# Kernel tuning notes

Hardware: AMD Instinct MI355X
Metric: run time of the kernel (lower is better)

## Reference

```python
import jax, jax.numpy as jnp
import numpy as np

NQ = 8          # n_qubits
NC = 4          # n_cycles of the angle encoder
PI = np.float32(np.pi)
LAYER_QUBITS = [[0, 1, 2, 3, 4, 5, 6, 7], [1, 3, 5, 7]]  # active qubits per conv layer
FINAL_QUBITS = [3, 7]                                    # active after last pooling
CX = jnp.array([[1, 0, 0, 0], [0, 1, 0, 0], [0, 0, 0, 1], [0, 0, 1, 0]], jnp.complex64)


def apply1(psi, U, q):
    """Apply 1-qubit gate U ((2,2) shared or (B,2,2) batched) on qubit q. psi: (B,2,...,2)."""
    psi = jnp.moveaxis(psi, 1 + q, -1)
    if U.ndim == 3:
        psi = jnp.einsum('bij,b...j->b...i', U, psi)
    else:
        psi = jnp.einsum('ij,...j->...i', U, psi)
    return jnp.moveaxis(psi, -1, 1 + q)


def apply2(psi, U, q0, q1):
    """Apply 2-qubit gate U (4,4) on (q0,q1); q0 is the more-significant wire."""
    psi = jnp.moveaxis(psi, (1 + q0, 1 + q1), (-2, -1))
    sh = psi.shape
    psi = jnp.einsum('ij,...j->...i', U, psi.reshape(sh[:-2] + (4,)))
    return jnp.moveaxis(psi.reshape(sh), (-2, -1), (1 + q0, 1 + q1))


def rz_mat(t):
    return jnp.array([[jnp.exp(-0.5j * t), 0.0], [0.0, jnp.exp(0.5j * t)]]).astype(jnp.complex64)


def ry_mat(t):
    c, s = jnp.cos(t / 2), jnp.sin(t / 2)
    return jnp.array([[c, -s], [s, c]]).astype(jnp.complex64)


def crx_mat(t):
    c = jnp.cos(t / 2).astype(jnp.complex64)
    s = jnp.sin(t / 2).astype(jnp.complex64)
    M = jnp.eye(4, dtype=jnp.complex64)
    return M.at[2, 2].set(c).at[3, 3].set(c).at[2, 3].set(-1j * s).at[3, 2].set(-1j * s)


def u3_mat(t, p, l):
    c, s = jnp.cos(t / 2), jnp.sin(t / 2)
    return jnp.array([[c + 0j, -jnp.exp(1j * l) * s],
                      [jnp.exp(1j * p) * s, jnp.exp(1j * (p + l)) * c]]).astype(jnp.complex64)


def expz(psi, q):
    """<Z_q> = P(q=0) - P(q=1)."""
    p = psi.real ** 2 + psi.imag ** 2
    p = jnp.moveaxis(p, 1 + q, 1).reshape(p.shape[0], 2, -1).sum(-1)
    return p[:, 0] - p[:, 1]


def encode(x):
    """Angle-encoding circuit (circuit_builder): NC cycles of RY(x) + CNOT ring."""
    B = x.shape[0]
    psi = jnp.zeros((B, 2 ** NQ), jnp.complex64).at[:, 0].set(1.0).reshape((B,) + (2,) * NQ)
    for c in range(NC):
        ang = x[:, c * NQ:(c + 1) * NQ]
        cc, ss = jnp.cos(ang / 2), jnp.sin(ang / 2)
        for q in range(NQ):
            U = jnp.stack([jnp.stack([cc[:, q], -ss[:, q]], -1),
                           jnp.stack([ss[:, q], cc[:, q]], -1)], -2).astype(jnp.complex64)
            psi = apply1(psi, U, q)
        for q in range(NQ):
            psi = apply2(psi, CX, q, (q + 1) % NQ)
    return psi


def forward(x, rz_p, ry_p, ry2_p, crx_p, u3_p, u3b_p, W1, b1, W2, b2):
    psi0 = encode(x)
    psi1 = psi0  # deepcopy of encoded state for the second feature map
    for layer in range(2):
        aq = LAYER_QUBITS[layer]
        n = len(aq)
        RZp, RYp, RY2p = rz_mat(rz_p[layer]), ry_mat(ry_p[layer]), ry_mat(ry2_p[layer])
        RZm, RZpl = rz_mat(-PI / 2), rz_mat(PI / 2)
        # circuit 1: ZNOTY-style conv blocks, even pairs then odd pairs
        for parity in (0, 1):
            for i in range(parity, n - 1, 2):
                qc, qt = aq[i], aq[i + 1]
                psi0 = apply1(psi0, RZm, qt)
                psi0 = apply2(psi0, CX, qt, qc)
                psi0 = apply1(psi0, RZp, qc)
                psi0 = apply1(psi0, RYp, qt)
                psi0 = apply2(psi0, CX, qc, qt)
                psi0 = apply1(psi0, RY2p, qt)
                psi0 = apply2(psi0, CX, qt, qc)
                psi0 = apply1(psi0, RZpl, qc)
        remain = [aq[i] for i in range(n) if i % 2 == 1]
        U3a = u3_mat(u3_p[layer, 0], u3_p[layer, 1], u3_p[layer, 2])
        for q in remain:
            psi0 = apply1(psi0, U3a, q)
        # circuit 2: CRX conv blocks, even pairs then odd pairs
        CRXp = crx_mat(crx_p[layer])
        for parity in (0, 1):
            for i in range(parity, n - 1, 2):
                psi1 = apply2(psi1, CRXp, aq[i], aq[i + 1])
        U3b = u3_mat(u3b_p[layer, 0], u3b_p[layer, 1], u3b_p[layer, 2])
        for q in remain:
            psi1 = apply1(psi1, U3b, q)
    xv = jnp.stack([expz(psi0, q) for q in FINAL_QUBITS], 1)  # (B,2)
    yv = jnp.stack([expz(psi1, q) for q in FINAL_QUBITS], 1)  # (B,2)
    feat = jnp.concatenate([xv, yv], 1)                       # (B,4)
    h = jnp.tanh(feat @ W1.T + b1)
    return jax.nn.sigmoid(h @ W2.T + b2)


def setup_inputs() -> dict:
    key = jax.random.key(0)
    ks = jax.random.split(key, 12)
    B = 8192
    return {
        'x': jax.random.normal(ks[0], (B, NC * NQ), jnp.float32),
        'rz_p': jax.random.normal(ks[1], (2,), jnp.float32) * 0.5,
        'ry_p': jax.random.normal(ks[2], (2,), jnp.float32) * 0.5,
        'ry2_p': jax.random.normal(ks[3], (2,), jnp.float32) * 0.5,
        'crx_p': jax.random.normal(ks[4], (2,), jnp.float32) * 0.5,
        'u3_p': jax.random.normal(ks[5], (2, 3), jnp.float32) * 0.5,
        'u3b_p': jax.random.normal(ks[6], (2, 3), jnp.float32) * 0.5,
        'W1': jax.random.normal(ks[7], (15, 4), jnp.float32) * 0.4,
        'b1': jax.random.normal(ks[8], (15,), jnp.float32) * 0.1,
        'W2': jax.random.normal(ks[9], (1, 15), jnp.float32) * 0.25,
        'b2': jax.random.normal(ks[10], (1,), jnp.float32) * 0.1,
    }


def reference(x, rz_p, ry_p, ry2_p, crx_p, u3_p, u3b_p, W1, b1, W2, b2):
    return forward(x, rz_p, ry_p, ry2_p, crx_p, u3_p, u3b_p, W1, b1, W2, b2)
```

## Files before the change

kernel.cpp:

```cpp
#include <hip/hip_runtime.h>

#define DEV __device__ __forceinline__


DEV int lpar(int lane, int m) { return __builtin_popcount(lane & m) & 1; }
constexpr int cpar(int v) { return (v ^ (v >> 1) ^ (v >> 2) ^ (v >> 3)) & 1; }

constexpr int TLm(int LM, int SM) { return (LM << 1) | (SM >> 3); }
constexpr int TSm(int SM) { return SM & 7; }

template<int LM, int SM, int LR, int SR>
DEV void ryr(float* p, float gc, float gs, int lane) {
  const float sg0 = lpar(lane, LR) ? gs : -gs;
  const float sg1 = -sg0;
  if constexpr (LM != 0) {
    float t[8];
    #pragma unroll
    for (int s = 0; s < 8; ++s) t[s] = __shfl_xor(p[s ^ SM], LM);
    #pragma unroll
    for (int s = 0; s < 8; ++s)
      p[s] = gc * p[s] + (cpar(s & SR) ? sg1 : sg0) * t[s];
  } else {
    constexpr int LOW = SM & (-SM);
    #pragma unroll
    for (int s = 0; s < 8; ++s) if (!(s & LOW)) {
      const int s1 = s ^ SM;
      float a = p[s], b = p[s1];
      float sg = cpar(s & SR) ? sg1 : sg0;
      p[s]  = gc * a + sg * b;
      p[s1] = gc * b - sg * a;
    }
  }
}

template<int LM, int SM, int LR, int SR>
DEV void u3_g(float* pr, float* pi, const float* u, int lane) {
  const bool hl = lpar(lane, LR);
  const float d0r = hl ? u[6] : u[0], d0i = hl ? u[7] : u[1];
  const float o0r = hl ? u[4] : u[2], o0i = hl ? u[5] : u[3];
  const float d1r = hl ? u[0] : u[6], d1i = hl ? u[1] : u[7];
  const float o1r = hl ? u[2] : u[4], o1i = hl ? u[3] : u[5];
  if constexpr (LM != 0) {
    float tr[8], ti[8];
    #pragma unroll
    for (int s = 0; s < 8; ++s) {
      tr[s] = __shfl_xor(pr[s ^ SM], LM);
      ti[s] = __shfl_xor(pi[s ^ SM], LM);
    }
    #pragma unroll
    for (int s = 0; s < 8; ++s) {
      const bool c1 = cpar(s & SR);
      const float dr = c1 ? d1r : d0r, di = c1 ? d1i : d0i;
      const float orr = c1 ? o1r : o0r, oi = c1 ? o1i : o0i;
      float ar = pr[s], ai = pi[s];
      pr[s] = dr*ar - di*ai + orr*tr[s] - oi*ti[s];
      pi[s] = dr*ai + di*ar + orr*ti[s] + oi*tr[s];
    }
  } else {
    constexpr int LOW = SM & (-SM);
    #pragma unroll
    for (int s = 0; s < 8; ++s) if (!(s & LOW)) {
      const int s1 = s ^ SM;
      const bool c1 = cpar(s & SR);
      const float dAr = c1 ? d1r : d0r, dAi = c1 ? d1i : d0i;
      const float oAr = c1 ? o1r : o0r, oAi = c1 ? o1i : o0i;
      const float dBr = c1 ? d0r : d1r, dBi = c1 ? d0i : d1i;
      const float oBr = c1 ? o0r : o1r, oBi = c1 ? o0i : o1i;
      float ar = pr[s], ai = pi[s], br = pr[s1], bi = pi[s1];
      pr[s]  = dAr*ar - dAi*ai + oAr*br - oAi*bi;
      pi[s]  = dAr*ai + dAi*ar + oAr*bi + oAi*br;
      pr[s1] = dBr*br - dBi*bi + oBr*ar - oBi*ai;
      pi[s1] = dBr*bi + dBi*br + oBr*ai + oBi*ar;
    }
  }
}

template<int LMt, int SMt, int LRc, int SRc>
DEV void crx_g(float* pr, float* pi, float c, float s_, int lane) {
  const bool hl = lpar(lane, LRc);
  const float cc0 = hl ? c : 1.0f, ss0 = hl ? s_ : 0.0f;
  const float cc1 = hl ? 1.0f : c, ss1 = hl ? 0.0f : s_;
  if constexpr (LMt != 0) {
    float tr[8], ti[8];
    #pragma unroll
    for (int s = 0; s < 8; ++s) {
      tr[s] = __shfl_xor(pr[s ^ SMt], LMt);
      ti[s] = __shfl_xor(pi[s ^ SMt], LMt);
    }
    #pragma unroll
    for (int s = 0; s < 8; ++s) {
      const bool c1 = cpar(s & SRc);
      const float cc = c1 ? cc1 : cc0, ss = c1 ? ss1 : ss0;
      float ar = pr[s], ai = pi[s];
      pr[s] = cc * ar + ss * ti[s];
      pi[s] = cc * ai - ss * tr[s];
    }
  } else {
    constexpr int LOW = SMt & (-SMt);
    #pragma unroll
    for (int s = 0; s < 8; ++s) if (!(s & LOW)) {
      const int s1 = s ^ SMt;
      const bool c1 = cpar(s & SRc);
      const float cc = c1 ? cc1 : cc0, ss = c1 ? ss1 : ss0;
      float ar = pr[s], ai = pi[s], br = pr[s1], bi = pi[s1];
      pr[s]  = cc * ar + ss * bi;
      pi[s]  = cc * ai - ss * br;
      pr[s1] = cc * br + ss * ai;
      pi[s1] = cc * bi - ss * ar;
    }
  }
}

#define U4CLASS(Q)                                                            \
  if constexpr (!(((SRc == 0) && (Q & 2)) || ((SRt == 0) && (Q & 1)))) {      \
    const int r1 = R ^ Q, r2 = r1 ^ 2;                                        \
    const float2 wd = w2[r1 * 4 + r1],       wo = w2[r1 * 4 + (r1 ^ 1)];      \
    const float2 vd = w2[r2 * 4 + r1],       vo = w2[r2 * 4 + (r1 ^ 1)];      \
    _Pragma("unroll")                                                         \
    for (int s = 0; s < 8; ++s)                                               \
      if (((cpar(s & SRc) << 1) | cpar(s & SRt)) == Q) {                      \
        float ar = pr[s], ai = pi[s], br = tr[s], bi = ti[s];                 \
        pr[s] = wd.x*ar - wd.y*ai + wo.x*br - wo.y*bi;                        \
        pi[s] = wd.x*ai + wd.y*ar + wo.x*bi + wo.y*br;                        \
        tr[s] = vd.x*ar - vd.y*ai + vo.x*br - vo.y*bi;                        \
        ti[s] = vd.x*ai + vd.y*ar + vo.x*bi + vo.y*br;                        \
      }                                                                       \
  }

template<int LMc, int SMc, int LMt, int SMt, int LRc, int SRc, int LRt, int SRt>
DEV void u4_g(float* pr, float* pi, const float2* w2, int lane) {
  const int R = (lpar(lane, LRc) << 1) | lpar(lane, LRt);
  float tr[8], ti[8];
  #pragma unroll
  for (int s = 0; s < 8; ++s) {
    float vr = pr[s ^ SMt], vi = pi[s ^ SMt];
    if constexpr (LMt != 0) { vr = __shfl_xor(vr, LMt); vi = __shfl_xor(vi, LMt); }
    tr[s] = vr; ti[s] = vi;
  }
  U4CLASS(0) U4CLASS(1) U4CLASS(2) U4CLASS(3)
  #pragma unroll
  for (int s = 0; s < 8; ++s) {
    float br = tr[s ^ SMc], bi = ti[s ^ SMc];
    if constexpr (LMc != 0) { br = __shfl_xor(br, LMc); bi = __shfl_xor(bi, LMc); }
    pr[s] += br; pi[s] += bi;
  }
}

template<int LMc,int SMc,int LMt,int SMt,int LRc,int SRc,int LRt,int SRt>
DEV void u4o(float* pr, float* pi, const float2* w2, int lane) {
  u4_g<TLm(LMc,SMc),TSm(SMc), TLm(LMt,SMt),TSm(SMt),
       TLm(LRc,SRc),TSm(SRc), TLm(LRt,SRt),TSm(SRt)>(pr, pi, w2, lane);
}
template<int LM,int SM,int LR,int SR>
DEV void u3o(float* pr, float* pi, const float* u, int lane) {
  u3_g<TLm(LM,SM),TSm(SM), TLm(LR,SR),TSm(SR)>(pr, pi, u, lane);
}
template<int LMt,int SMt,int LRc,int SRc>
DEV void crxo(float* pr, float* pi, float c, float s_, int lane) {
  crx_g<TLm(LMt,SMt),TSm(SMt), TLm(LRc,SRc),TSm(SRc)>(pr, pi, c, s_, lane);
}

DEV void u3_make(float t, float p, float l, float* u) {
  float c = __cosf(0.5f * t), s = __sinf(0.5f * t);
  float cp = __cosf(p), sp = __sinf(p);
  float cl = __cosf(l), sl = __sinf(l);
  float cpl = __cosf(p + l), spl = __sinf(p + l);
  u[0] = c;        u[1] = 0.0f;
  u[2] = -cl * s;  u[3] = -sl * s;
  u[4] = cp * s;   u[5] = sp * s;
  u[6] = cpl * c;  u[7] = spl * c;
}

DEV void expz_fin(const float* pr, const float* pi, int lane, float& z3, float& z7) {
  float t3 = 0.0f, t7 = 0.0f;
  #pragma unroll
  for (int s = 0; s < 8; ++s) {
    float p = pr[s] * pr[s] + pi[s] * pi[s];
    t7 += p;
    t3 += (s & 1) ? -p : p;
  }
  if (lpar(lane, 20)) { t3 = -t3; t7 = -t7; }
  #pragma unroll
  for (int m = 1; m < 32; m <<= 1) {
    t3 += __shfl_xor(t3, m);
    t7 += __shfl_xor(t7, m);
  }
  z3 = t3; z7 = t7;
}


__global__ __launch_bounds__(512, 2)
void qcnn_kernel(const float* __restrict__ x,
                 const float* __restrict__ rz_p, const float* __restrict__ ry_p,
                 const float* __restrict__ ry2_p, const float* __restrict__ crx_p,
                 const float* __restrict__ u3_p, const float* __restrict__ u3b_p,
                 const float* __restrict__ W1, const float* __restrict__ b1,
                 const float* __restrict__ W2, const float* __restrict__ b2,
                 float* __restrict__ out, int B) {
  __shared__ __align__(8) float cw[64];

  const int tid  = threadIdx.x;
  const int lane = tid & 63;
  const int wave = tid >> 6;
  const int sub  = lane & 15;
  const int half = lane >> 5;
  const int l5   = lane & 31;
  const int hb   = lane & 32;
  const int elem  = blockIdx.x * 16 + wave * 2 + half;
  const int elemc = elem < B ? elem : (B - 1);

  if (tid < 32) {
    const int lay = tid >> 4, e = tid & 15, i4 = e >> 2, j4 = e & 3;
    const int base = tid & 48;
    const float c45 = 0.70710678118654752f;
    float rz = rz_p[lay], ry = ry_p[lay], ry2 = ry2_p[lay];
    float mr = (i4 == j4) ? c45 : 0.0f;
    float mi = (i4 == j4) ? ((i4 & 1) ? -c45 : c45) : 0.0f;
    { int t = (i4 & 1) ? (i4 ^ 2) : i4; int src = base | (t << 2) | j4;
      mr = __shfl(mr, src); mi = __shfl(mi, src); }
    { float cz = __cosf(0.5f * rz), sz = __sinf(0.5f * rz);
      float di = (i4 & 2) ? sz : -sz;
      float nr = cz * mr - di * mi, ni = cz * mi + di * mr; mr = nr; mi = ni; }
    { float cy = __cosf(0.5f * ry), sy = __sinf(0.5f * ry);
      int src = base | ((i4 ^ 1) << 2) | j4;
      float orr = __shfl(mr, src), oii = __shfl(mi, src);
      float sg = (i4 & 1) ? sy : -sy;
      mr = cy * mr + sg * orr; mi = cy * mi + sg * oii; }
    { int t = (i4 & 2) ? (i4 ^ 1) : i4; int src = base | (t << 2) | j4;
      mr = __shfl(mr, src); mi = __shfl(mi, src); }
    { float cy = __cosf(0.5f * ry2), sy = __sinf(0.5f * ry2);
      int src = base | ((i4 ^ 1) << 2) | j4;
      float orr = __shfl(mr, src), oii = __shfl(mi, src);
      float sg = (i4 & 1) ? sy : -sy;
      mr = cy * mr + sg * orr; mi = cy * mi + sg * oii; }
    { int t = (i4 & 1) ? (i4 ^ 2) : i4; int src = base | (t << 2) | j4;
      mr = __shfl(mr, src); mi = __shfl(mi, src); }
    { float di = (i4 & 2) ? c45 : -c45;
      float nr = c45 * mr - di * mi, ni = c45 * mi + di * mr; mr = nr; mi = ni; }
    cw[(lay * 16 + e) * 2]     = mr;
    cw[(lay * 16 + e) * 2 + 1] = mi;
  }

  float2 aa = ((const float2*)x)[(size_t)elemc * 16 + sub];
  float ch0 = __cosf(0.5f * aa.x), sh0 = __sinf(0.5f * aa.x);
  float ch1 = __cosf(0.5f * aa.y), sh1 = __sinf(0.5f * aa.y);

  float cq[8], sq[8];
  #pragma unroll
  for (int q = 0; q < 8; ++q) {
    cq[q] = __shfl((q & 1) ? ch1 : ch0, hb | (q >> 1));
    sq[q] = __shfl((q & 1) ? sh1 : sh0, hb | (q >> 1));
  }

  float p[8];
  {
    float g = ((l5 & 16) ? sq[0] : cq[0]) * ((l5 & 8) ? sq[2] : cq[2]) *
              ((l5 & 4)  ? sq[4] : cq[4]) * ((l5 & 2) ? sq[6] : cq[6]) *
              ((l5 & 1)  ? sq[1] : cq[1]);
    #pragma unroll
    for (int s = 0; s < 8; ++s)
      p[s] = g * ((s & 4) ? sq[3] : cq[3]) * ((s & 2) ? sq[5] : cq[5]) *
                 ((s & 1) ? sq[7] : cq[7]);
  }

  #define ENC(k, LM, SM, LR, SR) {                                  \
    float gc = __shfl(((k) & 1) ? ch1 : ch0, hb | ((k) >> 1));      \
    float gs = __shfl(((k) & 1) ? sh1 : sh0, hb | ((k) >> 1));      \
    ryr<TLm(LM,SM), TSm(SM), TLm(LR,SR), TSm(SR)>(p, gc, gs, lane); }

  ENC(8,  8,8, 7,15)  ENC(9,  4,8, 8,8)   ENC(10, 4,4, 12,8)  ENC(11, 2,4, 12,12)
  ENC(12, 2,2, 14,12) ENC(13, 1,2, 14,14) ENC(14, 1,1, 15,14) ENC(15, 8,9, 15,15)
  ENC(16, 12,0, 8,15) ENC(17, 0,12, 15,7) ENC(18, 6,0, 3,15)  ENC(19, 0,6, 15,3)
  ENC(20, 3,0, 1,15)  ENC(21, 0,3, 15,1)  ENC(22, 9,8, 0,15)  ENC(23, 4,9, 15,0)
  ENC(24, 12,12, 2,10) ENC(25, 6,12, 7,8) ENC(26, 6,6, 4,7)   ENC(27, 3,6, 11,4)
  ENC(28, 3,3, 10,11)  ENC(29, 9,11, 5,10) ENC(30, 13,1, 5,5) ENC(31, 8,5, 10,5)
  #undef ENC

  float e_[8];
  #pragma unroll
  for (int s = 0; s < 8; ++s) e_[s] = p[s];

  __syncthreads();
  const float2* w0 = (const float2*)cw;
  const float2* w1 = ((const float2*)cw) + 16;

  float pi_[8];
  #pragma unroll
  for (int s = 0; s < 8; ++s) pi_[s] = 0.0f;

  u4o<10,0,  0,10, 8,10, 5,2 >(p, pi_, w0, lane);
  u4o<5,0,   0,5,  1,5,  10,1>(p, pi_, w0, lane);
  u4o<10,8,  4,10, 0,10, 5,0 >(p, pi_, w0, lane);
  u4o<5,4,   2,5,  0,5,  10,0>(p, pi_, w0, lane);
  u4o<0,10,  5,0,  5,2,  1,5 >(p, pi_, w0, lane);
  u4o<0,5,   10,8, 10,1, 0,10>(p, pi_, w0, lane);
  u4o<4,10,  5,4,  5,0,  0,5 >(p, pi_, w0, lane);
  {
    float ua[8]; u3_make(u3_p[0], u3_p[1], u3_p[2], ua);
    u3o<0,10, 5,2 >(p, pi_, ua, lane);
    u3o<0,5,  10,1>(p, pi_, ua, lane);
    u3o<4,10, 5,0 >(p, pi_, ua, lane);
    u3o<2,5,  10,0>(p, pi_, ua, lane);
  }
  u4o<0,10,  0,5,  5,2,  10,1>(p, pi_, w1, lane);
  u4o<4,10,  2,5,  5,0,  10,0>(p, pi_, w1, lane);
  u4o<0,5,   4,10, 10,1, 5,0 >(p, pi_, w1, lane);
  {
    float ua[8]; u3_make(u3_p[3], u3_p[4], u3_p[5], ua);
    u3o<0,5,  10,1>(p, pi_, ua, lane);
    u3o<2,5,  10,0>(p, pi_, ua, lane);
  }

  float f0, f1;
  expz_fin(p, pi_, lane, f0, f1);

  #pragma unroll
  for (int s = 0; s < 8; ++s) { p[s] = e_[s]; pi_[s] = 0.0f; }

  {
    float t = crx_p[0];
    float cc = __cosf(0.5f * t), ss = __sinf(0.5f * t);
    crxo<0,10, 8,10>(p, pi_, cc, ss, lane);
    crxo<0,5,  1,5 >(p, pi_, cc, ss, lane);
    crxo<4,10, 0,10>(p, pi_, cc, ss, lane);
    crxo<2,5,  0,5 >(p, pi_, cc, ss, lane);
    crxo<5,0,  5,2 >(p, pi_, cc, ss, lane);
    crxo<10,8, 10,1>(p, pi_, cc, ss, lane);
    crxo<5,4,  5,0 >(p, pi_, cc, ss, lane);
  }
  {
    float ub[8]; u3_make(u3b_p[0], u3b_p[1], u3b_p[2], ub);
    u3o<0,10, 5,2 >(p, pi_, ub, lane);
    u3o<0,5,  10,1>(p, pi_, ub, lane);
    u3o<4,10, 5,0 >(p, pi_, ub, lane);
    u3o<2,5,  10,0>(p, pi_, ub, lane);
  }
  {
    float t = crx_p[1];
    float cc = __cosf(0.5f * t), ss = __sinf(0.5f * t);
    crxo<0,5,  5,2 >(p, pi_, cc, ss, lane);
    crxo<2,5,  5,0 >(p, pi_, cc, ss, lane);
    crxo<4,10, 10,1>(p, pi_, cc, ss, lane);
  }
  {
    float ub[8]; u3_make(u3b_p[3], u3b_p[4], u3b_p[5], ub);
    u3o<0,5,  10,1>(p, pi_, ub, lane);
    u3o<2,5,  10,0>(p, pi_, ub, lane);
  }

  float f2, f3;
  expz_fin(p, pi_, lane, f2, f3);

  const int j = (l5 < 15) ? l5 : 0;
  float acc = W1[j * 4 + 0] * f0 + W1[j * 4 + 1] * f1 +
              W1[j * 4 + 2] * f2 + W1[j * 4 + 3] * f3 + b1[j];
  float e2 = __expf(2.0f * acc);
  float th = (e2 - 1.0f) / (e2 + 1.0f);
  float part = (l5 < 15) ? th * W2[j] : 0.0f;
  #pragma unroll
  for (int m = 1; m < 32; m <<= 1) part += __shfl_xor(part, m);

  if (l5 == 0 && elem < B) {
    float z = part + b2[0];
    out[elem] = 1.0f / (1.0f + __expf(-z));
  }
}

extern "C" void kernel_launch(void* const* d_in, const int* in_sizes, int n_in,
                              void* d_out, int out_size, void* d_ws, size_t ws_size,
                              hipStream_t stream) {
  (void)n_in; (void)out_size; (void)d_ws; (void)ws_size;
  const float* x     = (const float*)d_in[0];
  const float* rz_p  = (const float*)d_in[1];
  const float* ry_p  = (const float*)d_in[2];
  const float* ry2_p = (const float*)d_in[3];
  const float* crx_p = (const float*)d_in[4];
  const float* u3_p  = (const float*)d_in[5];
  const float* u3b_p = (const float*)d_in[6];
  const float* W1    = (const float*)d_in[7];
  const float* b1    = (const float*)d_in[8];
  const float* W2    = (const float*)d_in[9];
  const float* b2    = (const float*)d_in[10];
  float* out = (float*)d_out;

  const int B = in_sizes[0] / 32;
  const int blocks = (B + 15) / 16;
  qcnn_kernel<<<dim3(blocks), dim3(512), 0, stream>>>(
      x, rz_p, ry_p, ry2_p, crx_p, u3_p, u3b_p, W1, b1, W2, b2, out, B);
}
```

Baseline: 119.5 us.

## Fold single-qubit U3 gates into following two-qubit gate matrices per block

Precomputes fused 4x4 matrices per block in shared memory: the layer-1 U3 tensor-product is multiplied into the second-layer conv unitary, and the U3b pair is fused with the following CRX. Those fused matrices replace separate u3o/crxo applications in the per-element circuit, cutting the number of gate applications. It also hoists U3 and CRX trig setup into shared memory once per block. This adds more threads doing setup work before the sync, and correctness depends on the fused matrix ordering matching the original gate order.

```diff
diff --git a/kernel.cpp b/kernel.cpp
--- a/kernel.cpp
+++ b/kernel.cpp
@@ -198,6 +198,9 @@
                  const float* __restrict__ W2, const float* __restrict__ b2,
                  float* __restrict__ out, int B) {
   __shared__ __align__(8) float cw[64];
+  __shared__ __align__(8) float w1f[32];
+  __shared__ __align__(8) float cx2[32];
+  __shared__ float u3a2[8], u3b2[8], crxc[4];
 
   const int tid  = threadIdx.x;
   const int lane = tid & 63;
@@ -241,6 +244,57 @@
     cw[(lay * 16 + e) * 2 + 1] = mi;
   }
 
+  if (tid < 64) {
+    if (tid < 16) {
+      const int e = tid, i = e >> 2, j = e & 3;
+      float ua[8]; u3_make(u3_p[0], u3_p[1], u3_p[2], ua);
+      float sr = 0.0f, si = 0.0f;
+      #pragma unroll
+      for (int k = 0; k < 4; ++k) {
+        float wr = cw[(16 + i * 4 + k) * 2], wi = cw[(16 + i * 4 + k) * 2 + 1];
+        float ar = ua[((k >> 1) * 2 + (j >> 1)) * 2];
+        float ai = ua[((k >> 1) * 2 + (j >> 1)) * 2 + 1];
+        float br = ua[((k & 1) * 2 + (j & 1)) * 2];
+        float bi = ua[((k & 1) * 2 + (j & 1)) * 2 + 1];
+        float kr = ar * br - ai * bi, ki = ar * bi + ai * br;
+        sr += wr * kr - wi * ki; si += wr * ki + wi * kr;
+      }
+      w1f[e * 2] = sr; w1f[e * 2 + 1] = si;
+    } else if (tid < 32) {
+      const int e = tid - 16, i = e >> 2, j = e & 3;
+      float ub[8]; u3_make(u3b_p[0], u3b_p[1], u3b_p[2], ub);
+      float t1 = crx_p[1];
+      float cc = __cosf(0.5f * t1), ss = __sinf(0.5f * t1);
+      float kr[4], ki[4];
+      #pragma unroll
+      for (int k = 0; k < 4; ++k) {
+        float ar = ub[((k >> 1) * 2 + (j >> 1)) * 2];
+        float ai = ub[((k >> 1) * 2 + (j >> 1)) * 2 + 1];
+        float br = ub[((k & 1) * 2 + (j & 1)) * 2];
+        float bi = ub[((k & 1) * 2 + (j & 1)) * 2 + 1];
+        kr[k] = ar * br - ai * bi; ki[k] = ar * bi + ai * br;
+      }
+      float sr, si;
+      if (i == 0)      { sr = kr[0]; si = ki[0]; }
+      else if (i == 1) { sr = kr[1]; si = ki[1]; }
+      else if (i == 2) { sr = cc * kr[2] + ss * ki[3]; si = cc * ki[2] - ss * kr[3]; }
+      else             { sr = cc * kr[3] + ss * ki[2]; si = cc * ki[3] - ss * kr[2]; }
+      cx2[e * 2] = sr; cx2[e * 2 + 1] = si;
+    } else if (tid == 32) {
+      float ua[8]; u3_make(u3_p[3], u3_p[4], u3_p[5], ua);
+      #pragma unroll
+      for (int k = 0; k < 8; ++k) u3a2[k] = ua[k];
+    } else if (tid == 33) {
+      float ub[8]; u3_make(u3b_p[3], u3b_p[4], u3b_p[5], ub);
+      #pragma unroll
+      for (int k = 0; k < 8; ++k) u3b2[k] = ub[k];
+    } else if (tid == 34) {
+      float t0 = crx_p[0], t1 = crx_p[1];
+      crxc[0] = __cosf(0.5f * t0); crxc[1] = __sinf(0.5f * t0);
+      crxc[2] = __cosf(0.5f * t1); crxc[3] = __sinf(0.5f * t1);
+    }
+  }
+
   float2 aa = ((const float2*)x)[(size_t)elemc * 16 + sub];
   float ch0 = __cosf(0.5f * aa.x), sh0 = __sinf(0.5f * aa.x);
   float ch1 = __cosf(0.5f * aa.y), sh1 = __sinf(0.5f * aa.y);
@@ -281,8 +335,10 @@
   for (int s = 0; s < 8; ++s) e_[s] = p[s];
 
   __syncthreads();
-  const float2* w0 = (const float2*)cw;
-  const float2* w1 = ((const float2*)cw) + 16;
+  const float2* w0  = (const float2*)cw;
+  const float2* w1  = ((const float2*)cw) + 16;
+  const float2* wf  = (const float2*)w1f;
+  const float2* wc2 = (const float2*)cx2;
 
   float pi_[8];
   #pragma unroll
@@ -295,18 +351,13 @@
   u4o<0,10,  5,0,  5,2,  1,5 >(p, pi_, w0, lane);
   u4o<0,5,   10,8, 10,1, 0,10>(p, pi_, w0, lane);
   u4o<4,10,  5,4,  5,0,  0,5 >(p, pi_, w0, lane);
-  {
-    float ua[8]; u3_make(u3_p[0], u3_p[1], u3_p[2], ua);
-    u3o<0,10, 5,2 >(p, pi_, ua, lane);
-    u3o<0,5,  10,1>(p, pi_, ua, lane);
-    u3o<4,10, 5,0 >(p, pi_, ua, lane);
-    u3o<2,5,  10,0>(p, pi_, ua, lane);
-  }
-  u4o<0,10,  0,5,  5,2,  10,1>(p, pi_, w1, lane);
-  u4o<4,10,  2,5,  5,0,  10,0>(p, pi_, w1, lane);
+  u4o<0,10,  0,5,  5,2,  10,1>(p, pi_, wf, lane);
+  u4o<4,10,  2,5,  5,0,  10,0>(p, pi_, wf, lane);
   u4o<0,5,   4,10, 10,1, 5,0 >(p, pi_, w1, lane);
   {
-    float ua[8]; u3_make(u3_p[3], u3_p[4], u3_p[5], ua);
+    float ua[8];
+    #pragma unroll
+    for (int k = 0; k < 8; ++k) ua[k] = u3a2[k];
     u3o<0,5,  10,1>(p, pi_, ua, lane);
     u3o<2,5,  10,0>(p, pi_, ua, lane);
   }
@@ -318,8 +369,7 @@
   for (int s = 0; s < 8; ++s) { p[s] = e_[s]; pi_[s] = 0.0f; }
 
   {
-    float t = crx_p[0];
-    float cc = __cosf(0.5f * t), ss = __sinf(0.5f * t);
+    float cc = crxc[0], ss = crxc[1];
     crxo<0,10, 8,10>(p, pi_, cc, ss, lane);
     crxo<0,5,  1,5 >(p, pi_, cc, ss, lane);
     crxo<4,10, 0,10>(p, pi_, cc, ss, lane);
@@ -328,22 +378,16 @@
     crxo<10,8, 10,1>(p, pi_, cc, ss, lane);
     crxo<5,4,  5,0 >(p, pi_, cc, ss, lane);
   }
+  u4o<0,10,  0,5,  5,2,  10,1>(p, pi_, wc2, lane);
+  u4o<4,10,  2,5,  5,0,  10,0>(p, pi_, wc2, lane);
   {
-    float ub[8]; u3_make(u3b_p[0], u3b_p[1], u3b_p[2], ub);
-    u3o<0,10, 5,2 >(p, pi_, ub, lane);
-    u3o<0,5,  10,1>(p, pi_, ub, lane);
-    u3o<4,10, 5,0 >(p, pi_, ub, lane);
-    u3o<2,5,  10,0>(p, pi_, ub, lane);
+    float cc = crxc[2], ss = crxc[3];
+    crxo<4,10, 10,1>(p, pi_, cc, ss, lane);
   }
   {
-    float t = crx_p[1];
-    float cc = __cosf(0.5f * t), ss = __sinf(0.5f * t);
-    crxo<0,5,  5,2 >(p, pi_, cc, ss, lane);
-    crxo<2,5,  5,0 >(p, pi_, cc, ss, lane);
-    crxo<4,10, 10,1>(p, pi_, cc, ss, lane);
-  }
-  {
-    float ub[8]; u3_make(u3b_p[3], u3b_p[4], u3b_p[5], ub);
+    float ub[8];
+    #pragma unroll
+    for (int k = 0; k < 8; ++k) ub[k] = u3b2[k];
     u3o<0,5,  10,1>(p, pi_, ub, lane);
     u3o<2,5,  10,0>(p, pi_, ub, lane);
   }
```

Result: no change. 120.1 us (+0.6%).
